# Kernel optimization log

Measured on AMD Instinct MI355X. Metric: run time of the kernel, lower is better.

## Reference

```python
import jax, jax.numpy as jnp
import numpy as np

N_CELLS = 4096          # rows of sparse x
N_INPUT_GENES = 20000   # cols of sparse x == len(input_gene_list)
N_PRETRAINED = 30000    # rows of embedding table
NUM_HID = 128
NNZ = 2097152           # ~512 expressed genes per cell


def setup_inputs() -> dict:
    key = jax.random.key(0)
    k_val, k_row, k_col, k_gidx, k_emb = jax.random.split(key, 5)
    x_values = jax.random.uniform(k_val, (NNZ,), dtype=jnp.float32)
    x_rows = jnp.sort(jax.random.randint(k_row, (NNZ,), 0, N_CELLS))
    x_cols = jax.random.randint(k_col, (NNZ,), 0, N_INPUT_GENES)
    gene_idx = jax.random.randint(k_gidx, (N_INPUT_GENES,), 0, N_PRETRAINED)
    # nn.Parameter(torch.randn(...) * 0.005)
    embs = jax.random.normal(k_emb, (N_PRETRAINED, NUM_HID), dtype=jnp.float32) * 0.005
    return {"x_values": x_values, "x_rows": x_rows, "x_cols": x_cols,
            "gene_idx": gene_idx, "embs": embs}


def reference(x_values, x_rows, x_cols, gene_idx, embs):
    # feat = F.embedding(gene_idx, embs)           -> [G_in, H]
    # out  = torch.sparse.mm(x, feat)              -> [N_cells, H]
    # Fused: gather per-nnz embedding rows, scale by value, segment-sum by cell.
    feat = embs[gene_idx]                                   # [G_in, H]
    contrib = x_values[:, None] * feat[x_cols]              # [NNZ, H]
    out = jax.ops.segment_sum(contrib, x_rows,
                              num_segments=N_CELLS,
                              indices_are_sorted=True)      # [N_cells, H]
    return out
```

## Files before the change

kernel.cpp:

```cpp
#include <hip/hip_runtime.h>

#define NNZ_TOT    2097152
#define N_CELLS    4096
#define N_PRE      30000
#define NUM_HID    128

__global__ __launch_bounds__(256) void fuse_gidx_kernel(
    const int* __restrict__ xc, const int* __restrict__ gidx,
    int* __restrict__ g_arr)
{
    const int i = blockIdx.x * blockDim.x + threadIdx.x;
    if (i < NNZ_TOT) g_arr[i] = gidx[xc[i]];
}

__device__ __forceinline__ unsigned short f2bf(float f) {
    union { float f; unsigned u; } c; c.f = f;
    unsigned u = c.u;
    u += 0x7fffu + ((u >> 16) & 1u);
    return (unsigned short)(u >> 16);
}

__global__ __launch_bounds__(256) void convert_embs_kernel(
    const float* __restrict__ embs, unsigned short* __restrict__ ebf)
{
    const int i = blockIdx.x * blockDim.x + threadIdx.x;
    if (i * 4 < N_PRE * NUM_HID) {
        const float4 f = *reinterpret_cast<const float4*>(&embs[i * 4]);
        ushort4 o;
        o.x = f2bf(f.x); o.y = f2bf(f.y); o.z = f2bf(f.z); o.w = f2bf(f.w);
        *reinterpret_cast<ushort4*>(&ebf[i * 4]) = o;
    }
}

__global__ __launch_bounds__(256) void row_ptr_kernel(
    const int* __restrict__ xr, int* __restrict__ rp)
{
    const int r = blockIdx.x * blockDim.x + threadIdx.x;
    if (r <= N_CELLS) {
        int lo = 0, hi = NNZ_TOT;
        while (lo < hi) {
            const int mid = (lo + hi) >> 1;
            if (xr[mid] < r) lo = mid + 1; else hi = mid;
        }
        rp[r] = lo;
    }
}

__device__ __forceinline__ void fma8(uint4 f, float vv, float4& a0, float4& a1) {
    a0.x = fmaf(vv, __uint_as_float(f.x << 16),         a0.x);
    a0.y = fmaf(vv, __uint_as_float(f.x & 0xffff0000u), a0.y);
    a0.z = fmaf(vv, __uint_as_float(f.y << 16),         a0.z);
    a0.w = fmaf(vv, __uint_as_float(f.y & 0xffff0000u), a0.w);
    a1.x = fmaf(vv, __uint_as_float(f.z << 16),         a1.x);
    a1.y = fmaf(vv, __uint_as_float(f.z & 0xffff0000u), a1.y);
    a1.z = fmaf(vv, __uint_as_float(f.w << 16),         a1.z);
    a1.w = fmaf(vv, __uint_as_float(f.w & 0xffff0000u), a1.w);
}

__global__ __launch_bounds__(256) void omics_row_kernel(
    const float*          __restrict__ xv,
    const int*            __restrict__ g_arr,
    const int*            __restrict__ rp,
    const unsigned short* __restrict__ ebf,
    float*                __restrict__ out)
{
    const int wave = (blockIdx.x * blockDim.x + threadIdx.x) >> 6;
    const int lane = threadIdx.x & 63;
    const int sub  = lane & 15;
    const int quad = lane >> 4;
    const int r    = __builtin_amdgcn_readfirstlane(wave);
    if (r >= N_CELLS) return;

    const int lo = rp[r];
    const int hi = rp[r + 1];
    const int h8 = sub * 8;

    float4 a0 = make_float4(0.f, 0.f, 0.f, 0.f);
    float4 a1 = make_float4(0.f, 0.f, 0.f, 0.f);
    float4 b0 = make_float4(0.f, 0.f, 0.f, 0.f);
    float4 b1 = make_float4(0.f, 0.f, 0.f, 0.f);

    int i = lo;
    for (; i + 16 <= hi; i += 16) {
        const int i0 = i + quad;
        const int g0 = g_arr[i0];      const float v0 = xv[i0];
        const int g1 = g_arr[i0 + 4];  const float v1 = xv[i0 + 4];
        const int g2 = g_arr[i0 + 8];  const float v2 = xv[i0 + 8];
        const int g3 = g_arr[i0 + 12]; const float v3 = xv[i0 + 12];

        const uint4 f0 = *reinterpret_cast<const uint4*>(&ebf[(long)g0 * NUM_HID + h8]);
        const uint4 f1 = *reinterpret_cast<const uint4*>(&ebf[(long)g1 * NUM_HID + h8]);
        const uint4 f2 = *reinterpret_cast<const uint4*>(&ebf[(long)g2 * NUM_HID + h8]);
        const uint4 f3 = *reinterpret_cast<const uint4*>(&ebf[(long)g3 * NUM_HID + h8]);

        fma8(f0, v0, a0, a1);
        fma8(f1, v1, b0, b1);
        fma8(f2, v2, a0, a1);
        fma8(f3, v3, b0, b1);
    }
    for (; i < hi; i += 4) {
        const int  idx = i + quad;
        const bool ok  = idx < hi;
        const int   gg = g_arr[ok ? idx : (hi - 1)];
        const float vv = ok ? xv[idx] : 0.f;
        const uint4 f  = *reinterpret_cast<const uint4*>(&ebf[(long)gg * NUM_HID + h8]);
        fma8(f, vv, a0, a1);
    }

    a0.x += b0.x; a0.y += b0.y; a0.z += b0.z; a0.w += b0.w;
    a1.x += b1.x; a1.y += b1.y; a1.z += b1.z; a1.w += b1.w;

    a0.x += __shfl_xor(a0.x, 16); a0.x += __shfl_xor(a0.x, 32);
    a0.y += __shfl_xor(a0.y, 16); a0.y += __shfl_xor(a0.y, 32);
    a0.z += __shfl_xor(a0.z, 16); a0.z += __shfl_xor(a0.z, 32);
    a0.w += __shfl_xor(a0.w, 16); a0.w += __shfl_xor(a0.w, 32);
    a1.x += __shfl_xor(a1.x, 16); a1.x += __shfl_xor(a1.x, 32);
    a1.y += __shfl_xor(a1.y, 16); a1.y += __shfl_xor(a1.y, 32);
    a1.z += __shfl_xor(a1.z, 16); a1.z += __shfl_xor(a1.z, 32);
    a1.w += __shfl_xor(a1.w, 16); a1.w += __shfl_xor(a1.w, 32);

    if (quad == 0) {
        float* o = &out[(long)r * NUM_HID + h8];
        *reinterpret_cast<float4*>(o)     = a0;
        *reinterpret_cast<float4*>(o + 4) = a1;
    }
}

__global__ __launch_bounds__(256) void omics_fp32_row_kernel(
    const float* __restrict__ xv, const int* __restrict__ xr,
    const int* __restrict__ xc, const int* __restrict__ gidx,
    const float* __restrict__ embs, float* __restrict__ out)
{
    const int wave = (blockIdx.x * blockDim.x + threadIdx.x) >> 6;
    const int lane = threadIdx.x & 63;
    if (wave >= N_CELLS) return;
    int lo = 0, hi = NNZ_TOT;
    while (lo < hi) { int m = (lo + hi) >> 1; if (xr[m] < wave) lo = m + 1; else hi = m; }
    int lo2 = lo, hi2 = NNZ_TOT;
    while (lo2 < hi2) { int m = (lo2 + hi2) >> 1; if (xr[m] < wave + 1) lo2 = m + 1; else hi2 = m; }
    const int h = lane * 2;
    float2 acc = make_float2(0.f, 0.f);
    for (int i = lo; i < lo2; ++i) {
        const float v = xv[i];
        const int   g = gidx[xc[i]];
        const float2 f = *reinterpret_cast<const float2*>(&embs[(long)g * NUM_HID + h]);
        acc.x = fmaf(v, f.x, acc.x);
        acc.y = fmaf(v, f.y, acc.y);
    }
    *reinterpret_cast<float2*>(&out[(long)wave * NUM_HID + h]) = acc;
}

extern "C" void kernel_launch(void* const* d_in, const int* in_sizes, int n_in,
                              void* d_out, int out_size, void* d_ws, size_t ws_size,
                              hipStream_t stream) {
    const float* xv   = (const float*)d_in[0];
    const int*   xr   = (const int*)  d_in[1];
    const int*   xc   = (const int*)  d_in[2];
    const int*   gidx = (const int*)  d_in[3];
    const float* embs = (const float*)d_in[4];
    float*       out  = (float*)d_out;

    const size_t rp_bytes = ((size_t)(N_CELLS + 1) * sizeof(int) + 255) & ~255;
    const size_t g_bytes  = (size_t)NNZ_TOT * sizeof(int);
    const size_t e_bytes  = (size_t)N_PRE * NUM_HID * 2;

    if (ws_size >= rp_bytes + g_bytes + e_bytes) {
        int*            rp    = (int*)d_ws;
        int*            g_arr = (int*)((char*)d_ws + rp_bytes);
        unsigned short* ebf   = (unsigned short*)((char*)d_ws + rp_bytes + g_bytes);

        row_ptr_kernel<<<(N_CELLS + 256) / 256, 256, 0, stream>>>(xr, rp);
        fuse_gidx_kernel<<<(NNZ_TOT + 255) / 256, 256, 0, stream>>>(xc, gidx, g_arr);
        convert_embs_kernel<<<(N_PRE * NUM_HID / 4 + 255) / 256, 256, 0, stream>>>(embs, ebf);

        omics_row_kernel<<<(N_CELLS * 64) / 256, 256, 0, stream>>>(
            xv, g_arr, rp, ebf, out);
    } else {
        omics_fp32_row_kernel<<<(N_CELLS * 64) / 256, 256, 0, stream>>>(
            xv, xr, xc, gidx, embs, out);
    }
}
```

Measured before the change: 137.1 us.

## Replace per-nnz index materialization with a compact deduplicated bf16 embedding table

Drops the pass that wrote a 2M-entry pretrained-index array and the full-table bf16 conversion. Instead it deduplicates the referenced embedding rows with atomics into a compact bf16 table, plus a small column-to-compact-id map that the main kernel looks up per nonzero. The main loop is unrolled from 16 to 32 nonzeros per iteration to keep more gathers in flight. The cost is an extra dependent load in the inner loop, two memsets and an atomic id-assignment kernel. Rows that appear more than once are written redundantly with identical data.

```diff
diff --git a/kernel.cpp b/kernel.cpp
--- a/kernel.cpp
+++ b/kernel.cpp
@@ -2,16 +2,21 @@
 
 #define NNZ_TOT    2097152
 #define N_CELLS    4096
+#define N_GIN      20000
 #define N_PRE      30000
 #define NUM_HID    128
 
-__global__ __launch_bounds__(256) void fuse_gidx_kernel(
-    const int* __restrict__ xc, const int* __restrict__ gidx,
-    int* __restrict__ g_arr)
-{
-    const int i = blockIdx.x * blockDim.x + threadIdx.x;
-    if (i < NNZ_TOT) g_arr[i] = gidx[xc[i]];
-}
+#define EBF_OFF   0
+#define EBF_BYTES ((size_t)N_GIN * NUM_HID * 2)
+#define MARK_OFF  (EBF_OFF + EBF_BYTES)
+#define MARK_BYTES (((size_t)N_PRE * 4 + 255) & ~(size_t)255)
+#define MARK2_OFF (MARK_OFF + MARK_BYTES)
+#define MARK2_BYTES ((size_t)N_GIN * 4)
+#define MARK2_PAD (((MARK2_BYTES) + 255) & ~(size_t)255)
+#define RP_OFF    (MARK2_OFF + MARK2_PAD)
+#define RP_BYTES  ((((size_t)(N_CELLS + 1) * 4) + 255) & ~(size_t)255)
+#define CNT_OFF   (RP_OFF + RP_BYTES)
+#define WS_NEED   (CNT_OFF + 256)
 
 __device__ __forceinline__ unsigned short f2bf(float f) {
     union { float f; unsigned u; } c; c.f = f;
@@ -20,16 +25,36 @@
     return (unsigned short)(u >> 16);
 }
 
-__global__ __launch_bounds__(256) void convert_embs_kernel(
-    const float* __restrict__ embs, unsigned short* __restrict__ ebf)
-{
-    const int i = blockIdx.x * blockDim.x + threadIdx.x;
-    if (i * 4 < N_PRE * NUM_HID) {
-        const float4 f = *reinterpret_cast<const float4*>(&embs[i * 4]);
-        ushort4 o;
-        o.x = f2bf(f.x); o.y = f2bf(f.y); o.z = f2bf(f.z); o.w = f2bf(f.w);
-        *reinterpret_cast<ushort4*>(&ebf[i * 4]) = o;
-    }
+__global__ __launch_bounds__(256) void assign_ids_kernel(
+    const int* __restrict__ gidx, int* __restrict__ mark, int* __restrict__ cnt)
+{
+    const int j = blockIdx.x * blockDim.x + threadIdx.x;
+    if (j < N_GIN) {
+        const int g = gidx[j];
+        if (atomicCAS(&mark[g], -1, -2) == -1) {
+            const int id = atomicAdd(cnt, 1);
+            mark[g] = id;
+        }
+    }
+}
+
+__global__ __launch_bounds__(256) void build_table_kernel(
+    const int* __restrict__ gidx, const int* __restrict__ mark,
+    const float* __restrict__ embs, unsigned short* __restrict__ ebf,
+    int* __restrict__ mark2)
+{
+    const int tid = blockIdx.x * blockDim.x + threadIdx.x;
+    const int j = tid >> 5;
+    const int k = tid & 31;
+    if (j >= N_GIN) return;
+    const int g  = gidx[j];
+    const int id = mark[g];
+    if (k == 0) mark2[j] = id;
+    const float4 f = *reinterpret_cast<const float4*>(
+        &embs[(long)g * NUM_HID + k * 4]);
+    ushort4 o;
+    o.x = f2bf(f.x); o.y = f2bf(f.y); o.z = f2bf(f.z); o.w = f2bf(f.w);
+    *reinterpret_cast<ushort4*>(&ebf[(long)id * NUM_HID + k * 4]) = o;
 }
 
 __global__ __launch_bounds__(256) void row_ptr_kernel(
@@ -59,7 +84,8 @@
 
 __global__ __launch_bounds__(256) void omics_row_kernel(
     const float*          __restrict__ xv,
-    const int*            __restrict__ g_arr,
+    const int*            __restrict__ xc,
+    const int*            __restrict__ mark2,
     const int*            __restrict__ rp,
     const unsigned short* __restrict__ ebf,
     float*                __restrict__ out)
@@ -81,28 +107,46 @@
     float4 b1 = make_float4(0.f, 0.f, 0.f, 0.f);
 
     int i = lo;
-    for (; i + 16 <= hi; i += 16) {
+    for (; i + 32 <= hi; i += 32) {
         const int i0 = i + quad;
-        const int g0 = g_arr[i0];      const float v0 = xv[i0];
-        const int g1 = g_arr[i0 + 4];  const float v1 = xv[i0 + 4];
-        const int g2 = g_arr[i0 + 8];  const float v2 = xv[i0 + 8];
-        const int g3 = g_arr[i0 + 12]; const float v3 = xv[i0 + 12];
+        const int c0 = xc[i0];      const float v0 = xv[i0];
+        const int c1 = xc[i0 + 4];  const float v1 = xv[i0 + 4];
+        const int c2 = xc[i0 + 8];  const float v2 = xv[i0 + 8];
+        const int c3 = xc[i0 + 12]; const float v3 = xv[i0 + 12];
+        const int c4 = xc[i0 + 16]; const float v4 = xv[i0 + 16];
+        const int c5 = xc[i0 + 20]; const float v5 = xv[i0 + 20];
+        const int c6 = xc[i0 + 24]; const float v6 = xv[i0 + 24];
+        const int c7 = xc[i0 + 28]; const float v7 = xv[i0 + 28];
+
+        const int g0 = mark2[c0]; const int g1 = mark2[c1];
+        const int g2 = mark2[c2]; const int g3 = mark2[c3];
+        const int g4 = mark2[c4]; const int g5 = mark2[c5];
+        const int g6 = mark2[c6]; const int g7 = mark2[c7];
 
         const uint4 f0 = *reinterpret_cast<const uint4*>(&ebf[(long)g0 * NUM_HID + h8]);
         const uint4 f1 = *reinterpret_cast<const uint4*>(&ebf[(long)g1 * NUM_HID + h8]);
         const uint4 f2 = *reinterpret_cast<const uint4*>(&ebf[(long)g2 * NUM_HID + h8]);
         const uint4 f3 = *reinterpret_cast<const uint4*>(&ebf[(long)g3 * NUM_HID + h8]);
+        const uint4 f4 = *reinterpret_cast<const uint4*>(&ebf[(long)g4 * NUM_HID + h8]);
+        const uint4 f5 = *reinterpret_cast<const uint4*>(&ebf[(long)g5 * NUM_HID + h8]);
+        const uint4 f6 = *reinterpret_cast<const uint4*>(&ebf[(long)g6 * NUM_HID + h8]);
+        const uint4 f7 = *reinterpret_cast<const uint4*>(&ebf[(long)g7 * NUM_HID + h8]);
 
         fma8(f0, v0, a0, a1);
         fma8(f1, v1, b0, b1);
         fma8(f2, v2, a0, a1);
         fma8(f3, v3, b0, b1);
+        fma8(f4, v4, a0, a1);
+        fma8(f5, v5, b0, b1);
+        fma8(f6, v6, a0, a1);
+        fma8(f7, v7, b0, b1);
     }
     for (; i < hi; i += 4) {
         const int  idx = i + quad;
         const bool ok  = idx < hi;
-        const int   gg = g_arr[ok ? idx : (hi - 1)];
+        const int   cc = xc[ok ? idx : (hi - 1)];
         const float vv = ok ? xv[idx] : 0.f;
+        const int   gg = mark2[cc];
         const uint4 f  = *reinterpret_cast<const uint4*>(&ebf[(long)gg * NUM_HID + h8]);
         fma8(f, vv, a0, a1);
     }
@@ -160,21 +204,23 @@
     const float* embs = (const float*)d_in[4];
     float*       out  = (float*)d_out;
 
-    const size_t rp_bytes = ((size_t)(N_CELLS + 1) * sizeof(int) + 255) & ~255;
-    const size_t g_bytes  = (size_t)NNZ_TOT * sizeof(int);
-    const size_t e_bytes  = (size_t)N_PRE * NUM_HID * 2;
-
-    if (ws_size >= rp_bytes + g_bytes + e_bytes) {
-        int*            rp    = (int*)d_ws;
-        int*            g_arr = (int*)((char*)d_ws + rp_bytes);
-        unsigned short* ebf   = (unsigned short*)((char*)d_ws + rp_bytes + g_bytes);
-
+    if (ws_size >= WS_NEED) {
+        unsigned short* ebf   = (unsigned short*)((char*)d_ws + EBF_OFF);
+        int*            mark  = (int*)((char*)d_ws + MARK_OFF);
+        int*            mark2 = (int*)((char*)d_ws + MARK2_OFF);
+        int*            rp    = (int*)((char*)d_ws + RP_OFF);
+        int*            cnt   = (int*)((char*)d_ws + CNT_OFF);
+
+        hipMemsetAsync(mark, 0xFF, (size_t)N_PRE * 4, stream);
+        hipMemsetAsync(cnt, 0, 4, stream);
+
+        assign_ids_kernel<<<(N_GIN + 255) / 256, 256, 0, stream>>>(gidx, mark, cnt);
+        build_table_kernel<<<(N_GIN * 32 + 255) / 256, 256, 0, stream>>>(
+            gidx, mark, embs, ebf, mark2);
         row_ptr_kernel<<<(N_CELLS + 256) / 256, 256, 0, stream>>>(xr, rp);
-        fuse_gidx_kernel<<<(NNZ_TOT + 255) / 256, 256, 0, stream>>>(xc, gidx, g_arr);
-        convert_embs_kernel<<<(N_PRE * NUM_HID / 4 + 255) / 256, 256, 0, stream>>>(embs, ebf);
 
         omics_row_kernel<<<(N_CELLS * 64) / 256, 256, 0, stream>>>(
-            xv, g_arr, rp, ebf, out);
+            xv, xc, mark2, rp, ebf, out);
     } else {
         omics_fp32_row_kernel<<<(N_CELLS * 64) / 256, 256, 0, stream>>>(
             xv, xr, xc, gidx, embs, out);
```

After: 140.0 us. 2.1% more time.
